# Optimization experiments

Measured on AMD Instinct MI355X. Metric: run time of the kernel, lower is better.

Reference implementation:

```python
import jax, jax.numpy as jnp
import numpy as np
import math

D = 1024
H = 16
C = D // H
EPS = 1e-5

def layernorm(x, g, b):
    mu = jnp.mean(x, axis=-1, keepdims=True)
    var = jnp.mean(jnp.square(x - mu), axis=-1, keepdims=True)
    return (x - mu) * jax.lax.rsqrt(var + EPS) * g + b

def setup_inputs() -> dict:
    key = jax.random.key(0)
    ks = jax.random.split(key, 12)
    s = 1.0 / math.sqrt(D)
    inp = {
        "x": jax.random.normal(ks[0], (4, 2048, D), dtype=jnp.float32),
        "src_mask": jnp.ones((4, 2048), dtype=bool),
        "Wk": jax.random.normal(ks[1], (D, D), dtype=jnp.float32) * s,
        "Wq": jax.random.normal(ks[2], (D, D), dtype=jnp.float32) * s,
        "Wv": jax.random.normal(ks[3], (D, D), dtype=jnp.float32) * s,
        "Wfc": jax.random.normal(ks[4], (D, D), dtype=jnp.float32) * s,
        "bfc": jnp.zeros((D,), dtype=jnp.float32),
        "g1": jnp.ones((D,), dtype=jnp.float32),
        "b1": jnp.zeros((D,), dtype=jnp.float32),
        "g2": jnp.ones((D,), dtype=jnp.float32),
        "b2": jnp.zeros((D,), dtype=jnp.float32),
        "W1": jax.random.normal(ks[5], (D, 4 * D), dtype=jnp.float32) * s,
        "bf1": jnp.zeros((4 * D,), dtype=jnp.float32),
        "W2": jax.random.normal(ks[6], (4 * D, D), dtype=jnp.float32) * (1.0 / math.sqrt(4 * D)),
        "bf2": jnp.zeros((D,), dtype=jnp.float32),
    }
    return inp

def reference(x, src_mask, Wk, Wq, Wv, Wfc, bfc, g1, b1, g2, b2, W1, bf1, W2, bf2):
    b, s, _ = x.shape
    xl = layernorm(x, g1, b1)
    # self-attention (src_mask is unused in the original module)
    k = (xl @ Wk).reshape(b, s, H, C).transpose(0, 2, 1, 3)  # bhsc
    q = (xl @ Wq).reshape(b, s, H, C).transpose(0, 2, 1, 3)
    v = (xl @ Wv).reshape(b, s, H, C).transpose(0, 2, 1, 3)
    # NOTE: original multiplies by sqrt(c) (not divide) -- faithful quirk
    scores = jnp.einsum('bhqc,bhkc->bhqk', q, k) * math.sqrt(C)
    attn = jax.nn.softmax(scores, axis=-1)
    o = jnp.einsum('bhqk,bhkc->bhqc', attn, v)
    o = o.transpose(0, 2, 1, 3).reshape(b, s, D)
    ka = o @ Wfc + bfc
    x = ka + x
    xl2 = layernorm(x, g2, b2)
    ff = jax.nn.relu(xl2 @ W1 + bf1) @ W2 + bf2
    return ff + x
```

## Files before the change

kernel.cpp:

```cpp
#include <hip/hip_runtime.h>
#include <hip/hip_bf16.h>
#include <math.h>


typedef __hip_bfloat16 bf16_t;
typedef __bf16 bf16x8 __attribute__((ext_vector_type(8)));
typedef float f32x4 __attribute__((ext_vector_type(4)));

#define LN_EPS 1e-5f
#define QSCALE 11.541560327111707f
#define RESCALE_THR 100.0f
#define M0_PRIOR 275.0f

__device__ __forceinline__ void async_copy16(const bf16_t* g, bf16_t* l) {
  __builtin_amdgcn_global_load_lds(
      (const __attribute__((address_space(1))) void*)g,
      (__attribute__((address_space(3))) void*)l,
      16 , 0 , 0 );
}

__device__ __forceinline__ void split_bf16(float v, bf16_t& hi, bf16_t& lo) {
  hi = __float2bfloat16(v);
  lo = __float2bfloat16(v - __bfloat162float(hi));
}

__device__ __forceinline__ unsigned pack_bf16(float lo, float hi) {
  bf16_t a = __float2bfloat16(lo), b = __float2bfloat16(hi);
  unsigned short ua, ub;
  __builtin_memcpy(&ua, &a, 2);
  __builtin_memcpy(&ub, &b, 2);
  return (unsigned)ua | ((unsigned)ub << 16);
}

template<bool SPLIT>
__global__ __launch_bounds__(256) void ln_kernel(
    const float* __restrict__ x, const float* __restrict__ g,
    const float* __restrict__ b, bf16_t* __restrict__ out_hi,
    bf16_t* __restrict__ out_lo)
{
  const int row = blockIdx.x;
  const int tid = threadIdx.x;
  const float4 v = *(const float4*)(x + (size_t)row * 1024 + tid * 4);
  float s  = v.x + v.y + v.z + v.w;
  float ss = v.x * v.x + v.y * v.y + v.z * v.z + v.w * v.w;
  for (int off = 32; off > 0; off >>= 1) {
    s  += __shfl_down(s, off);
    ss += __shfl_down(ss, off);
  }
  __shared__ float sb[4], ssb[4];
  const int wave = tid >> 6, lane = tid & 63;
  if (lane == 0) { sb[wave] = s; ssb[wave] = ss; }
  __syncthreads();
  const float tot  = sb[0] + sb[1] + sb[2] + sb[3];
  const float tots = ssb[0] + ssb[1] + ssb[2] + ssb[3];
  const float mu   = tot * (1.0f / 1024.0f);
  const float var  = tots * (1.0f / 1024.0f) - mu * mu;
  const float rstd = rsqrtf(var + LN_EPS);
  const float4 gv = *(const float4*)(g + tid * 4);
  const float4 bv = *(const float4*)(b + tid * 4);
  float y[4] = {(v.x - mu) * rstd * gv.x + bv.x,
                (v.y - mu) * rstd * gv.y + bv.y,
                (v.z - mu) * rstd * gv.z + bv.z,
                (v.w - mu) * rstd * gv.w + bv.w};
  bf16_t hi[4] __attribute__((aligned(8)));
  bf16_t lo[4] __attribute__((aligned(8)));
  #pragma unroll
  for (int i = 0; i < 4; i++) split_bf16(y[i], hi[i], lo[i]);
  uint2 ph, pl;
  __builtin_memcpy(&ph, hi, 8);
  *(uint2*)(out_hi + (size_t)row * 1024 + tid * 4) = ph;
  if (SPLIT) {
    __builtin_memcpy(&pl, lo, 8);
    *(uint2*)(out_lo + (size_t)row * 1024 + tid * 4) = pl;
  }
}

__global__ __launch_bounds__(256) void wtrans_all_kernel(
    const float* __restrict__ Wq, const float* __restrict__ Wk,
    const float* __restrict__ Wv, const float* __restrict__ Wfc,
    const float* __restrict__ W1, const float* __restrict__ W2,
    bf16_t* __restrict__ WqkH, bf16_t* __restrict__ WqkL,
    bf16_t* __restrict__ WvT, bf16_t* __restrict__ WfcT,
    bf16_t* __restrict__ W1T, bf16_t* __restrict__ W2T)
{
  const int id = blockIdx.x;
  const float* W; bf16_t* DH; bf16_t* DL = nullptr;
  int K, N, n0, k0;
  if (id < 4096) {
    K = 1024; N = 1024;
    const int local = id & 1023;
    n0 = (local & 31) * 32; k0 = (local >> 5) * 32;
    if (id < 1024)      { W = Wq;  DH = WqkH;                 DL = WqkL; }
    else if (id < 2048) { W = Wk;  DH = WqkH + 1024 * 1024;   DL = WqkL + 1024 * 1024; }
    else if (id < 3072) { W = Wv;  DH = WvT; }
    else                { W = Wfc; DH = WfcT; }
  } else if (id < 8192) {
    const int local = id - 4096;
    K = 1024; N = 4096; W = W1; DH = W1T;
    n0 = (local & 127) * 32; k0 = (local >> 7) * 32;
  } else {
    const int local = id - 8192;
    K = 4096; N = 1024; W = W2; DH = W2T;
    n0 = (local & 31) * 32; k0 = (local >> 5) * 32;
  }
  __shared__ float t[32][33];
  const int tx = threadIdx.x & 31, ty = threadIdx.x >> 5;
  #pragma unroll
  for (int r = ty; r < 32; r += 8)
    t[r][tx] = W[(size_t)(k0 + r) * N + n0 + tx];
  __syncthreads();
  #pragma unroll
  for (int r = ty; r < 32; r += 8) {
    const float v = t[tx][r];
    bf16_t hi, lo;
    split_bf16(v, hi, lo);
    DH[(size_t)(n0 + r) * K + k0 + tx] = hi;
    if (DL) DL[(size_t)(n0 + r) * K + k0 + tx] = lo;
  }
}

template<bool BIAS, bool RELU, bool RESID, bool OUTBF>
__global__ __launch_bounds__(256) void gemm_kernel(
    const bf16_t* __restrict__ A, const bf16_t* __restrict__ BT,
    const float* __restrict__ bias, const float* __restrict__ resid,
    float* __restrict__ outF, bf16_t* __restrict__ outB,
    int M, int N, int K)
{
  __shared__ __align__(16) bf16_t As[128 * 64];
  __shared__ __align__(16) bf16_t Bs[128 * 64];
  const int nblk = N >> 7;
  const int wg = (blockIdx.x & 7) * (gridDim.x >> 3) + (blockIdx.x >> 3);
  const int bm = wg / nblk;
  const int bn = wg % nblk;
  const int tid  = threadIdx.x;
  const int wave = tid >> 6;
  const int lane = tid & 63;
  const int l15  = lane & 15;
  const int quad = lane >> 4;
  const int wm = wave >> 1, wn = wave & 1;

  const int srow = lane >> 3;
  const int schunk = (lane & 7) ^ srow;
  const bf16_t* aG = A  + (size_t)(bm * 128 + wave * 32 + srow) * K + schunk * 8;
  const bf16_t* bG = BT + (size_t)(bn * 128 + wave * 32 + srow) * K + schunk * 8;

  f32x4 acc[4][4];
  #pragma unroll
  for (int i = 0; i < 4; i++)
    #pragma unroll
    for (int j = 0; j < 4; j++) acc[i][j] = (f32x4){0.f, 0.f, 0.f, 0.f};

  const int rsw = l15 & 7;

  for (int kt = 0; kt < K; kt += 64) {
    #pragma unroll
    for (int j = 0; j < 4; j++) {
      async_copy16(aG + kt + (size_t)(j * 8) * K, &As[(wave * 32 + j * 8) * 64]);
      async_copy16(bG + kt + (size_t)(j * 8) * K, &Bs[(wave * 32 + j * 8) * 64]);
    }
    __syncthreads();
    #pragma unroll
    for (int ko = 0; ko < 2; ko++) {
      bf16x8 af[4], bfr[4];
      #pragma unroll
      for (int i = 0; i < 4; i++)
        af[i]  = *(const bf16x8*)&As[(wm * 64 + i * 16 + l15) * 64 +
                                     (((ko * 4 + quad) ^ rsw) * 8)];
      #pragma unroll
      for (int j = 0; j < 4; j++)
        bfr[j] = *(const bf16x8*)&Bs[(wn * 64 + j * 16 + l15) * 64 +
                                     (((ko * 4 + quad) ^ rsw) * 8)];
      #pragma unroll
      for (int i = 0; i < 4; i++)
        #pragma unroll
        for (int j = 0; j < 4; j++)
          acc[i][j] = __builtin_amdgcn_mfma_f32_16x16x32_bf16(af[i], bfr[j], acc[i][j], 0, 0, 0);
    }
    __syncthreads();
  }

  const int gm0 = bm * 128 + wm * 64 + quad * 4;
  const int gn0 = bn * 128 + wn * 64 + l15;
  #pragma unroll
  for (int i = 0; i < 4; i++) {
    #pragma unroll
    for (int j = 0; j < 4; j++) {
      const int gn = gn0 + j * 16;
      const float bz = BIAS ? bias[gn] : 0.0f;
      #pragma unroll
      for (int r = 0; r < 4; r++) {
        const int gm = gm0 + i * 16 + r;
        float v = acc[i][j][r] + bz;
        if (RESID) v += resid[(size_t)gm * N + gn];
        if (RELU)  v = fmaxf(v, 0.0f);
        if (OUTBF) outB[(size_t)gm * N + gn] = __float2bfloat16(v);
        else       outF[(size_t)gm * N + gn] = v;
      }
    }
  }
}

__global__ __launch_bounds__(256) void gemm_split_kernel(
    const bf16_t* __restrict__ Ah, const bf16_t* __restrict__ Al,
    const bf16_t* __restrict__ Bh, const bf16_t* __restrict__ Bl,
    bf16_t* __restrict__ out_hi, bf16_t* __restrict__ out_lo,
    int M, int N, int K)
{
  __shared__ __align__(16) bf16_t AsH[128 * 32];
  __shared__ __align__(16) bf16_t AsL[128 * 32];
  __shared__ __align__(16) bf16_t BsH[128 * 32];
  __shared__ __align__(16) bf16_t BsL[128 * 32];
  const int nblk = N >> 7;
  const int wg = (blockIdx.x & 7) * (gridDim.x >> 3) + (blockIdx.x >> 3);
  const int bm = wg / nblk;
  const int bn = wg % nblk;
  const int tid  = threadIdx.x;
  const int wave = tid >> 6;
  const int lane = tid & 63;
  const int l15  = lane & 15;
  const int quad = lane >> 4;
  const int wm = wave >> 1, wn = wave & 1;

  const int srow = lane >> 2;
  const int schunk = (lane & 3) ^ ((lane >> 3) & 3);
  const size_t aOff = (size_t)(bm * 128 + wave * 32 + srow) * K + schunk * 8;
  const size_t bOff = (size_t)(bn * 128 + wave * 32 + srow) * K + schunk * 8;
  const int ldsOff0 = (wave * 32) * 32;
  const int ldsOff1 = (wave * 32 + 16) * 32;

  f32x4 acc[4][4];
  #pragma unroll
  for (int i = 0; i < 4; i++)
    #pragma unroll
    for (int j = 0; j < 4; j++) acc[i][j] = (f32x4){0.f, 0.f, 0.f, 0.f};

  const int rsw = (l15 >> 1) & 3;

  for (int kt = 0; kt < K; kt += 32) {
    async_copy16(Ah + aOff + kt, &AsH[ldsOff0]);
    async_copy16(Ah + aOff + kt + (size_t)16 * K, &AsH[ldsOff1]);
    async_copy16(Al + aOff + kt, &AsL[ldsOff0]);
    async_copy16(Al + aOff + kt + (size_t)16 * K, &AsL[ldsOff1]);
    async_copy16(Bh + bOff + kt, &BsH[ldsOff0]);
    async_copy16(Bh + bOff + kt + (size_t)16 * K, &BsH[ldsOff1]);
    async_copy16(Bl + bOff + kt, &BsL[ldsOff0]);
    async_copy16(Bl + bOff + kt + (size_t)16 * K, &BsL[ldsOff1]);
    __syncthreads();
    bf16x8 afH[4], afL[4], bfH[4], bfL[4];
    #pragma unroll
    for (int i = 0; i < 4; i++) {
      const int o = (wm * 64 + i * 16 + l15) * 32 + ((quad ^ rsw) * 8);
      afH[i] = *(const bf16x8*)&AsH[o];
      afL[i] = *(const bf16x8*)&AsL[o];
    }
    #pragma unroll
    for (int j = 0; j < 4; j++) {
      const int o = (wn * 64 + j * 16 + l15) * 32 + ((quad ^ rsw) * 8);
      bfH[j] = *(const bf16x8*)&BsH[o];
      bfL[j] = *(const bf16x8*)&BsL[o];
    }
    #pragma unroll
    for (int i = 0; i < 4; i++)
      #pragma unroll
      for (int j = 0; j < 4; j++) {
        acc[i][j] = __builtin_amdgcn_mfma_f32_16x16x32_bf16(afH[i], bfH[j], acc[i][j], 0, 0, 0);
        acc[i][j] = __builtin_amdgcn_mfma_f32_16x16x32_bf16(afH[i], bfL[j], acc[i][j], 0, 0, 0);
        acc[i][j] = __builtin_amdgcn_mfma_f32_16x16x32_bf16(afL[i], bfH[j], acc[i][j], 0, 0, 0);
      }
    __syncthreads();
  }

  const int gm0 = bm * 128 + wm * 64 + quad * 4;
  const int gn0 = bn * 128 + wn * 64 + l15;
  #pragma unroll
  for (int i = 0; i < 4; i++)
    #pragma unroll
    for (int j = 0; j < 4; j++) {
      const int gn = gn0 + j * 16;
      const float scale = (gn < 1024) ? QSCALE : 1.0f;
      #pragma unroll
      for (int r = 0; r < 4; r++) {
        const int gm = gm0 + i * 16 + r;
        bf16_t hi, lo;
        split_bf16(acc[i][j][r] * scale, hi, lo);
        out_hi[(size_t)gm * N + gn] = hi;
        out_lo[(size_t)gm * N + gn] = lo;
      }
    }
}

__global__ __launch_bounds__(256) void attn_kernel(
    const bf16_t* __restrict__ qkH,
    const bf16_t* __restrict__ qkL,
    const bf16_t* __restrict__ vT,
    bf16_t* __restrict__ o)
{
  const int lin   = blockIdx.x;
  const int slice = (lin & 7) * 8 + ((lin >> 3) & 7);
  const int qt    = lin >> 6;
  const int h     = slice & 15;
  const int b     = slice >> 4;
  const int wave = threadIdx.x >> 6;
  const int lane = threadIdx.x & 63;
  const int l15  = lane & 15;
  const int quad = lane >> 4;
  const int sw   = l15 & 7;
  const int qrowA = qt * 128 + wave * 32;
  const int qrowB = qrowA + 16;

  __shared__ __align__(16) bf16_t SMEM[20480];
  bf16_t* pw = SMEM + 16384 + wave * 1024;
  unsigned* pw32 = (unsigned*)pw;

  const size_t tok0 = (size_t)b * 2048;
  const size_t qoffA = (tok0 + qrowA + l15) * 2048 + h * 64;
  const size_t qoffB = (tok0 + qrowB + l15) * 2048 + h * 64;
  const bf16x8 aA0H = *(const bf16x8*)(qkH + qoffA + quad * 8);
  const bf16x8 aA1H = *(const bf16x8*)(qkH + qoffA + 32 + quad * 8);
  const bf16x8 aA0L = *(const bf16x8*)(qkL + qoffA + quad * 8);
  const bf16x8 aA1L = *(const bf16x8*)(qkL + qoffA + 32 + quad * 8);
  const bf16x8 aB0H = *(const bf16x8*)(qkH + qoffB + quad * 8);
  const bf16x8 aB1H = *(const bf16x8*)(qkH + qoffB + 32 + quad * 8);
  const bf16x8 aB0L = *(const bf16x8*)(qkL + qoffB + quad * 8);
  const bf16x8 aB1L = *(const bf16x8*)(qkL + qoffB + 32 + quad * 8);

  const int kOff = 1024 + h * 64;
  const int rsub = lane >> 3;
  const int csw  = (lane & 7) ^ rsub;

  const bf16_t* vRow[4];
  #pragma unroll
  for (int c = 0; c < 4; c++)
    vRow[c] = vT + (size_t)(h * 64 + c * 16 + l15) * 8192 + tok0 + quad * 8;

  const int psw = (l15 >> 1) & 3;
  const int wbaseA = l15 * 16 + (quad & 1) * 2;
  const int wbaseB = wbaseA + 256;

  float negMA = -M0_PRIOR, negMB = -M0_PRIOR;
  float lsumA = 0.f, lsumB = 0.f;
  f32x4 OfA[4], OfB[4];
  #pragma unroll
  for (int c = 0; c < 4; c++) {
    OfA[c] = (f32x4){0.f, 0.f, 0.f, 0.f};
    OfB[c] = (f32x4){0.f, 0.f, 0.f, 0.f};
  }

  #pragma unroll
  for (int j = 0; j < 2; j++) {
    const int row0 = wave * 16 + j * 8;
    const size_t krow = tok0 + row0 + rsub;
    async_copy16(qkH + krow * 2048 + kOff + csw * 8, &SMEM[row0 * 64]);
    async_copy16(qkL + krow * 2048 + kOff + csw * 8, &SMEM[8192 + row0 * 64]);
  }
  __syncthreads();

  for (int i = 0; i < 32; i++) {
    const int kbase = i * 64;
    const int co = (i & 1) * 4096;
    const int no = 4096 - co;
    if (i < 31) {
      #pragma unroll
      for (int j = 0; j < 2; j++) {
        const int row0 = wave * 16 + j * 8;
        const size_t krow = tok0 + kbase + 64 + row0 + rsub;
        async_copy16(qkH + krow * 2048 + kOff + csw * 8, &SMEM[no + row0 * 64]);
        async_copy16(qkL + krow * 2048 + kOff + csw * 8, &SMEM[8192 + no + row0 * 64]);
      }
    }
    const bf16_t* KhC = SMEM + co;
    const bf16_t* KlC = SMEM + 8192 + co;

    #pragma unroll
    for (int half = 0; half < 2; half++) {
      const int koff = kbase + half * 32;
      bf16x8 bv[4];
      #pragma unroll
      for (int c = 0; c < 4; c++)
        bv[c] = *(const bf16x8*)(vRow[c] + koff);

      #pragma unroll
      for (int tl = 0; tl < 2; tl++) {
        const int t = half * 2 + tl;
        const int base = (t * 16 + l15) * 64;
        const bf16x8 bh0 = *(const bf16x8*)&KhC[base + ((quad) ^ sw) * 8];
        const bf16x8 bh1 = *(const bf16x8*)&KhC[base + ((4 + quad) ^ sw) * 8];
        const bf16x8 bl0 = *(const bf16x8*)&KlC[base + ((quad) ^ sw) * 8];
        const bf16x8 bl1 = *(const bf16x8*)&KlC[base + ((4 + quad) ^ sw) * 8];
        f32x4 accA = (f32x4){negMA, negMA, negMA, negMA};
        f32x4 accB = (f32x4){negMB, negMB, negMB, negMB};
        __builtin_amdgcn_s_setprio(1);
        accA = __builtin_amdgcn_mfma_f32_16x16x32_bf16(bh0, aA0H, accA, 0, 0, 0);
        accA = __builtin_amdgcn_mfma_f32_16x16x32_bf16(bh1, aA1H, accA, 0, 0, 0);
        accA = __builtin_amdgcn_mfma_f32_16x16x32_bf16(bl0, aA0H, accA, 0, 0, 0);
        accA = __builtin_amdgcn_mfma_f32_16x16x32_bf16(bl1, aA1H, accA, 0, 0, 0);
        accA = __builtin_amdgcn_mfma_f32_16x16x32_bf16(bh0, aA0L, accA, 0, 0, 0);
        accA = __builtin_amdgcn_mfma_f32_16x16x32_bf16(bh1, aA1L, accA, 0, 0, 0);
        accB = __builtin_amdgcn_mfma_f32_16x16x32_bf16(bh0, aB0H, accB, 0, 0, 0);
        accB = __builtin_amdgcn_mfma_f32_16x16x32_bf16(bh1, aB1H, accB, 0, 0, 0);
        accB = __builtin_amdgcn_mfma_f32_16x16x32_bf16(bl0, aB0H, accB, 0, 0, 0);
        accB = __builtin_amdgcn_mfma_f32_16x16x32_bf16(bl1, aB1H, accB, 0, 0, 0);
        accB = __builtin_amdgcn_mfma_f32_16x16x32_bf16(bh0, aB0L, accB, 0, 0, 0);
        accB = __builtin_amdgcn_mfma_f32_16x16x32_bf16(bh1, aB1L, accB, 0, 0, 0);
        __builtin_amdgcn_s_setprio(0);

        float pmax = fmaxf(fmaxf(fmaxf(accA[0], accA[1]), fmaxf(accA[2], accA[3])),
                           fmaxf(fmaxf(accB[0], accB[1]), fmaxf(accB[2], accB[3])));
        if (!__all(pmax <= RESCALE_THR)) {
          float mA = fmaxf(fmaxf(accA[0], accA[1]), fmaxf(accA[2], accA[3]));
          float mB = fmaxf(fmaxf(accB[0], accB[1]), fmaxf(accB[2], accB[3]));
          mA = fmaxf(mA, __shfl_xor(mA, 16)); mB = fmaxf(mB, __shfl_xor(mB, 16));
          mA = fmaxf(mA, __shfl_xor(mA, 32)); mB = fmaxf(mB, __shfl_xor(mB, 32));
          const float sA = fmaxf(mA, 0.0f);
          const float sB = fmaxf(mB, 0.0f);
          const float fA = __builtin_amdgcn_exp2f(-sA);
          const float fB = __builtin_amdgcn_exp2f(-sB);
          negMA -= sA;  negMB -= sB;
          lsumA *= fA;  lsumB *= fB;
          #pragma unroll
          for (int r = 0; r < 4; r++) {
            accA[r] -= sA;  accB[r] -= sB;
          }
          #pragma unroll
          for (int r = 0; r < 4; r++) {
            const int src = quad * 20 + r;
            const float fqA = __shfl(fA, src);
            const float fqB = __shfl(fB, src);
            #pragma unroll
            for (int c = 0; c < 4; c++) { OfA[c][r] *= fqA; OfB[c][r] *= fqB; }
          }
          if (tl == 1) {
            asm volatile("" ::: "memory");
            const int slot0 = (quad >> 1) ^ psw;
            const int iA = wbaseA + slot0 * 4;
            const int iB = wbaseB + slot0 * 4;
            #pragma unroll
            for (int j2 = 0; j2 < 2; j2++) {
              unsigned ua = pw32[iA + j2], ub = pw32[iB + j2];
              float a0 = __uint_as_float((ua & 0xffffu) << 16) * fA;
              float a1 = __uint_as_float(ua & 0xffff0000u) * fA;
              float b0 = __uint_as_float((ub & 0xffffu) << 16) * fB;
              float b1 = __uint_as_float(ub & 0xffff0000u) * fB;
              pw32[iA + j2] = pack_bf16(a0, a1);
              pw32[iB + j2] = pack_bf16(b0, b1);
            }
            asm volatile("" ::: "memory");
          }
        }

        const float pA0 = __builtin_amdgcn_exp2f(accA[0]);
        const float pA1 = __builtin_amdgcn_exp2f(accA[1]);
        const float pA2 = __builtin_amdgcn_exp2f(accA[2]);
        const float pA3 = __builtin_amdgcn_exp2f(accA[3]);
        const float pB0 = __builtin_amdgcn_exp2f(accB[0]);
        const float pB1 = __builtin_amdgcn_exp2f(accB[1]);
        const float pB2 = __builtin_amdgcn_exp2f(accB[2]);
        const float pB3 = __builtin_amdgcn_exp2f(accB[3]);
        lsumA += (pA0 + pA1) + (pA2 + pA3);
        lsumB += (pB0 + pB1) + (pB2 + pB3);
        const int slot = ((tl * 2) + (quad >> 1)) ^ psw;
        const int iA = wbaseA + slot * 4;
        const int iB = wbaseB + slot * 4;
        pw32[iA]     = pack_bf16(pA0, pA1);
        pw32[iA + 1] = pack_bf16(pA2, pA3);
        pw32[iB]     = pack_bf16(pB0, pB1);
        pw32[iB + 1] = pack_bf16(pB2, pB3);
      }

      asm volatile("" ::: "memory");

      const bf16x8 paA = *(const bf16x8*)&pw[l15 * 32 + ((quad ^ psw) * 8)];
      const bf16x8 paB = *(const bf16x8*)&pw[(16 + l15) * 32 + ((quad ^ psw) * 8)];
      __builtin_amdgcn_s_setprio(1);
      #pragma unroll
      for (int c = 0; c < 4; c++) {
        OfA[c] = __builtin_amdgcn_mfma_f32_16x16x32_bf16(paA, bv[c], OfA[c], 0, 0, 0);
        OfB[c] = __builtin_amdgcn_mfma_f32_16x16x32_bf16(paB, bv[c], OfB[c], 0, 0, 0);
      }
      __builtin_amdgcn_s_setprio(0);

      asm volatile("" ::: "memory");
    }
    __syncthreads();
  }

  float lrowA = lsumA, lrowB = lsumB;
  lrowA += __shfl_xor(lrowA, 16); lrowB += __shfl_xor(lrowB, 16);
  lrowA += __shfl_xor(lrowA, 32); lrowB += __shfl_xor(lrowB, 32);

  bf16_t* opA = o + (tok0 + qrowA) * 1024 + h * 64;
  bf16_t* opB = o + (tok0 + qrowB) * 1024 + h * 64;
  #pragma unroll
  for (int r = 0; r < 4; r++) {
    const int src = quad * 20 + r;
    const float rdA = 1.0f / __shfl(lrowA, src);
    const float rdB = 1.0f / __shfl(lrowB, src);
    #pragma unroll
    for (int c = 0; c < 4; c++) {
      opA[(size_t)(quad * 4 + r) * 1024 + c * 16 + l15] =
          __float2bfloat16(OfA[c][r] * rdA);
      opB[(size_t)(quad * 4 + r) * 1024 + c * 16 + l15] =
          __float2bfloat16(OfB[c][r] * rdB);
    }
  }
}

extern "C" void kernel_launch(void* const* d_in, const int* in_sizes, int n_in,
                              void* d_out, int out_size, void* d_ws, size_t ws_size,
                              hipStream_t stream)
{
  (void)in_sizes; (void)n_in; (void)out_size; (void)ws_size;
  const float* x   = (const float*)d_in[0];
  const float* Wk  = (const float*)d_in[2];
  const float* Wq  = (const float*)d_in[3];
  const float* Wv  = (const float*)d_in[4];
  const float* Wfc = (const float*)d_in[5];
  const float* bfc = (const float*)d_in[6];
  const float* g1  = (const float*)d_in[7];
  const float* b1  = (const float*)d_in[8];
  const float* g2  = (const float*)d_in[9];
  const float* b2  = (const float*)d_in[10];
  const float* W1  = (const float*)d_in[11];
  const float* bf1 = (const float*)d_in[12];
  const float* W2  = (const float*)d_in[13];
  const float* bf2 = (const float*)d_in[14];
  float* out = (float*)d_out;

  char* ws = (char*)d_ws;
  bf16_t* xl_hi  = (bf16_t*)(ws + (0ull   << 20));
  bf16_t* oAtt   = xl_hi;
  bf16_t* xl_lo  = (bf16_t*)(ws + (16ull  << 20));
  bf16_t* vT     = xl_lo;
  bf16_t* xl2    = xl_lo;
  bf16_t* qk_hi  = (bf16_t*)(ws + (32ull  << 20));
  bf16_t* qk_lo  = (bf16_t*)(ws + (64ull  << 20));
  bf16_t* h1     = qk_hi;
  float*  x2     = (float*) (ws + (112ull << 20));
  bf16_t* Wqk_hi = (bf16_t*)(ws + (144ull << 20));
  bf16_t* Wqk_lo = (bf16_t*)(ws + (148ull << 20));
  bf16_t* WvT    = (bf16_t*)(ws + (152ull << 20));
  bf16_t* WfcT   = (bf16_t*)(ws + (154ull << 20));
  bf16_t* W1T    = (bf16_t*)(ws + (156ull << 20));
  bf16_t* W2T    = (bf16_t*)(ws + (164ull << 20));

  const dim3 blk(256);

  wtrans_all_kernel<<<12288, blk, 0, stream>>>(
      Wq, Wk, Wv, Wfc, W1, W2, Wqk_hi, Wqk_lo, WvT, WfcT, W1T, W2T);

  ln_kernel<true><<<8192, blk, 0, stream>>>(x, g1, b1, xl_hi, xl_lo);

  gemm_split_kernel<<<64 * 16, blk, 0, stream>>>(
      xl_hi, xl_lo, Wqk_hi, Wqk_lo, qk_hi, qk_lo, 8192, 2048, 1024);

  gemm_kernel<false, false, false, true><<<8 * 64, blk, 0, stream>>>(
      WvT, xl_hi, nullptr, nullptr, nullptr, vT, 1024, 8192, 1024);

  attn_kernel<<<dim3(1024), blk, 0, stream>>>(qk_hi, qk_lo, vT, oAtt);

  gemm_kernel<true, false, true, false><<<64 * 8, blk, 0, stream>>>(
      oAtt, WfcT, bfc, x, x2, nullptr, 8192, 1024, 1024);

  ln_kernel<false><<<8192, blk, 0, stream>>>(x2, g2, b2, xl2, nullptr);

  gemm_kernel<true, true, false, true><<<64 * 32, blk, 0, stream>>>(
      xl2, W1T, bf1, nullptr, nullptr, h1, 8192, 4096, 1024);

  gemm_kernel<true, false, true, false><<<64 * 8, blk, 0, stream>>>(
      h1, W2T, bf2, x2, out, nullptr, 8192, 1024, 4096);
}
```

Measured before the change: 643.0 us.

## Triple-buffer GEMM LDS tiles with async prefetch two k-steps ahead

The GEMM main loop moves from a single 64-wide K tile loaded and consumed with two barriers per iteration to a three-stage ring of 32-wide K tiles. Global-to-LDS async copies for step t+2 are issued while step t computes, using vmcnt waits and a single barrier per step. The goal is to hide global-load latency behind MFMA work. In exchange it adds more loop iterations with less compute per barrier, a different XOR swizzle, and hand-tuned waitcnt that must match the number of outstanding copies.

```diff
diff --git a/kernel.cpp b/kernel.cpp
--- a/kernel.cpp
+++ b/kernel.cpp
@@ -126,8 +126,8 @@
     float* __restrict__ outF, bf16_t* __restrict__ outB,
     int M, int N, int K)
 {
-  __shared__ __align__(16) bf16_t As[128 * 64];
-  __shared__ __align__(16) bf16_t Bs[128 * 64];
+  __shared__ __align__(16) bf16_t As[3][128 * 32];
+  __shared__ __align__(16) bf16_t Bs[3][128 * 32];
   const int nblk = N >> 7;
   const int wg = (blockIdx.x & 7) * (gridDim.x >> 3) + (blockIdx.x >> 3);
   const int bm = wg / nblk;
@@ -139,10 +139,10 @@
   const int quad = lane >> 4;
   const int wm = wave >> 1, wn = wave & 1;
 
-  const int srow = lane >> 3;
-  const int schunk = (lane & 7) ^ srow;
-  const bf16_t* aG = A  + (size_t)(bm * 128 + wave * 32 + srow) * K + schunk * 8;
-  const bf16_t* bG = BT + (size_t)(bn * 128 + wave * 32 + srow) * K + schunk * 8;
+  const int gch = (tid & 3) ^ ((tid >> 3) & 3);
+  const bf16_t* aG = A  + (size_t)(bm * 128 + (tid >> 2)) * K + gch * 8;
+  const bf16_t* bG = BT + (size_t)(bn * 128 + (tid >> 2)) * K + gch * 8;
+  const int ldsW = wave * 512;
 
   f32x4 acc[4][4];
   #pragma unroll
@@ -150,33 +150,50 @@
     #pragma unroll
     for (int j = 0; j < 4; j++) acc[i][j] = (f32x4){0.f, 0.f, 0.f, 0.f};
 
-  const int rsw = l15 & 7;
-
-  for (int kt = 0; kt < K; kt += 64) {
-    #pragma unroll
-    for (int j = 0; j < 4; j++) {
-      async_copy16(aG + kt + (size_t)(j * 8) * K, &As[(wave * 32 + j * 8) * 64]);
-      async_copy16(bG + kt + (size_t)(j * 8) * K, &Bs[(wave * 32 + j * 8) * 64]);
-    }
-    __syncthreads();
-    #pragma unroll
-    for (int ko = 0; ko < 2; ko++) {
-      bf16x8 af[4], bfr[4];
-      #pragma unroll
-      for (int i = 0; i < 4; i++)
-        af[i]  = *(const bf16x8*)&As[(wm * 64 + i * 16 + l15) * 64 +
-                                     (((ko * 4 + quad) ^ rsw) * 8)];
+  const int rsw = (l15 >> 1) & 3;
+  const int T = K >> 5;
+
+  #pragma unroll
+  for (int s = 0; s < 2; s++) {
+    async_copy16(aG + (size_t)(s * 64) * K,      &As[0][s * 2048 + ldsW]);
+    async_copy16(bG + (size_t)(s * 64) * K,      &Bs[0][s * 2048 + ldsW]);
+    async_copy16(aG + (size_t)(s * 64) * K + 32, &As[1][s * 2048 + ldsW]);
+    async_copy16(bG + (size_t)(s * 64) * K + 32, &Bs[1][s * 2048 + ldsW]);
+  }
+
+  int bi = 0;
+  for (int t = 0; t < T; t++) {
+    if (t < T - 1) asm volatile("s_waitcnt vmcnt(4)" ::: "memory");
+    else           asm volatile("s_waitcnt vmcnt(0)" ::: "memory");
+    __builtin_amdgcn_s_barrier();
+    asm volatile("" ::: "memory");
+
+    if (t + 2 < T) {
+      int sb = bi + 2; if (sb >= 3) sb -= 3;
+      const int kof = (t + 2) * 32;
+      #pragma unroll
+      for (int s = 0; s < 2; s++) {
+        async_copy16(aG + (size_t)(s * 64) * K + kof, &As[sb][s * 2048 + ldsW]);
+        async_copy16(bG + (size_t)(s * 64) * K + kof, &Bs[sb][s * 2048 + ldsW]);
+      }
+    }
+
+    bf16x8 af[4], bfr[4];
+    #pragma unroll
+    for (int i = 0; i < 4; i++)
+      af[i]  = *(const bf16x8*)&As[bi][(wm * 64 + i * 16 + l15) * 32 +
+                                       ((quad ^ rsw) * 8)];
+    #pragma unroll
+    for (int j = 0; j < 4; j++)
+      bfr[j] = *(const bf16x8*)&Bs[bi][(wn * 64 + j * 16 + l15) * 32 +
+                                       ((quad ^ rsw) * 8)];
+    #pragma unroll
+    for (int i = 0; i < 4; i++)
       #pragma unroll
       for (int j = 0; j < 4; j++)
-        bfr[j] = *(const bf16x8*)&Bs[(wn * 64 + j * 16 + l15) * 64 +
-                                     (((ko * 4 + quad) ^ rsw) * 8)];
-      #pragma unroll
-      for (int i = 0; i < 4; i++)
-        #pragma unroll
-        for (int j = 0; j < 4; j++)
-          acc[i][j] = __builtin_amdgcn_mfma_f32_16x16x32_bf16(af[i], bfr[j], acc[i][j], 0, 0, 0);
-    }
-    __syncthreads();
+        acc[i][j] = __builtin_amdgcn_mfma_f32_16x16x32_bf16(af[i], bfr[j], acc[i][j], 0, 0, 0);
+
+    bi = (bi == 2) ? 0 : bi + 1;
   }
 
   const int gm0 = bm * 128 + wm * 64 + quad * 4;
```

Measured after the change: 661.3 us. 2.8% more time.
